# Kernel optimization log

Hardware: AMD Instinct MI355X
Metric: run time of the kernel (lower is better)

Reference implementation:

```python
import jax, jax.numpy as jnp
import numpy as np

B, S, D, H = 2, 2048, 1024, 16
DK = D // H


def setup_inputs() -> dict:
    key = jax.random.key(0)
    ks = jax.random.split(key, 12)
    scale = 0.02
    inp = {
        "query": jax.random.normal(ks[0], (B, S, D), jnp.float32),
        "key_": jax.random.normal(ks[1], (B, S, D), jnp.float32),
        "value": jax.random.normal(ks[2], (B, S, D), jnp.float32),
        # causal mask; masked_fill where mask == 0
        "mask": jnp.tril(jnp.ones((S, S), jnp.int32))[None, None, :, :],
        # torch Linear weights are [out, in]; y = x @ W.T + b
        "Wq": jax.random.normal(ks[3], (D, D), jnp.float32) * scale,
        "bq": jax.random.normal(ks[4], (D,), jnp.float32) * scale,
        "Wk": jax.random.normal(ks[5], (D, D), jnp.float32) * scale,
        "bk": jax.random.normal(ks[6], (D,), jnp.float32) * scale,
        "Wv": jax.random.normal(ks[7], (D, D), jnp.float32) * scale,
        "bv": jax.random.normal(ks[8], (D,), jnp.float32) * scale,
        "Wo": jax.random.normal(ks[9], (D, D), jnp.float32) * scale,
        "bo": jax.random.normal(ks[10], (D,), jnp.float32) * scale,
    }
    return inp


def reference(query, key_, value, mask, Wq, bq, Wk, bk, Wv, bv, Wo, bo):
    # projections (torch Linear: x @ W.T + b)
    Q = query @ Wq.T + bq
    K = key_ @ Wk.T + bk
    V = value @ Wv.T + bv
    # [B, S, D] -> [B, H, S, DK]
    Q = Q.reshape(B, S, H, DK).transpose(0, 2, 1, 3)
    K = K.reshape(B, S, H, DK).transpose(0, 2, 1, 3)
    V = V.reshape(B, S, H, DK).transpose(0, 2, 1, 3)
    scores = jnp.einsum("bhqd,bhkd->bhqk", Q, K) / jnp.sqrt(jnp.float32(DK))
    scores = jnp.where(mask == 0, jnp.float32(-1e9), scores)
    attn = jax.nn.softmax(scores, axis=-1)
    # dropout is identity in eval mode
    context = jnp.einsum("bhqk,bhkd->bhqd", attn, V)
    context = context.transpose(0, 2, 1, 3).reshape(B, S, D)
    output = context @ Wo.T + bo
    return (output, attn)
```

## Files before the change

kernel.cpp:

```cpp
#include <hip/hip_runtime.h>
#include <hip/hip_bf16.h>

#define BB 2
#define SS 2048
#define DD 1024
#define HH 16

typedef __attribute__((ext_vector_type(8))) short bf16x8;
typedef __attribute__((ext_vector_type(4))) float f32x4;
typedef __attribute__((ext_vector_type(4))) unsigned int u32x4;
typedef __attribute__((ext_vector_type(2))) unsigned int u32x2;

__device__ inline unsigned short f2bf(float f) {
  unsigned int u = __float_as_uint(f);
  u += 0x7fff + ((u >> 16) & 1);
  return (unsigned short)(u >> 16);
}

__device__ inline void gll16(const void* g, void* l) {
  __builtin_amdgcn_global_load_lds(
      (const __attribute__((address_space(1))) unsigned int*)g,
      (__attribute__((address_space(3))) unsigned int*)l, 16, 0, 0);
}

__device__ inline int swz(int row, int col) {
  return row * 64 + ((((col >> 3) + row + (row >> 3)) & 7) << 3) + (col & 7);
}

__global__ void convert_all(const float* __restrict__ q, const float* __restrict__ k,
                            const float* __restrict__ v, const float* __restrict__ wq,
                            const float* __restrict__ wk, const float* __restrict__ wv,
                            const float* __restrict__ wo, unsigned short* __restrict__ dst) {
  int gi = blockIdx.x * 256 + threadIdx.x;
  long base = (long)gi * 4;
  if (base >= 16777216L) return;
  const float* src;
  long off;
  if (base < 12582912L) {
    int a = (int)(base >> 22);
    off = base & 4194303L;
    src = (a == 0) ? q : (a == 1 ? k : v);
  } else {
    long wb = base - 12582912L;
    int a = (int)(wb >> 20);
    off = wb & 1048575L;
    src = (a == 0) ? wq : (a == 1 ? wk : (a == 2 ? wv : wo));
  }
  const float4 f = *(const float4*)(src + off);
  ushort4 o;
  o.x = f2bf(f.x); o.y = f2bf(f.y); o.z = f2bf(f.z); o.w = f2bf(f.w);
  *(ushort4*)(dst + base) = o;
}

template <int OUT_F32>
__global__ __launch_bounds__(256, 3) void gemm_bt(const unsigned short* __restrict__ Aall,
                                                  const unsigned short* __restrict__ Wall,
                                                  const float* __restrict__ b0,
                                                  const float* __restrict__ b1,
                                                  const float* __restrict__ b2,
                                                  void* __restrict__ Call) {
  __shared__ unsigned short As[128 * 64];
  __shared__ unsigned short Bs[128 * 64];
  const int tid = threadIdx.x;
  const int lane = tid & 63;
  const int w = tid >> 6;
  const int wm = w >> 1, wn = w & 1;
  const int z = blockIdx.z;
  const int m0 = blockIdx.y * 128;
  const int n0 = blockIdx.x * 128;
  const unsigned short* A = Aall + (long)z * 4194304;
  const unsigned short* W = Wall + (long)z * 1048576;
  const float* bias = (z == 0) ? b0 : (z == 1 ? b1 : b2);
  const int r = lane & 15, g = lane >> 4;
  const int lrow = lane >> 3;
  const int lcol = (lane & 7) * 8;

  f32x4 acc[4][4];
#pragma unroll
  for (int i = 0; i < 4; i++)
#pragma unroll
    for (int j = 0; j < 4; j++) acc[i][j] = (f32x4){0.f, 0.f, 0.f, 0.f};

  for (int kt = 0; kt < 16; kt++) {
    const int k0 = kt * 64;
#pragma unroll
    for (int t = 0; t < 4; t++) {
      int row = w * 32 + t * 8 + lrow;
      gll16(A + (long)(m0 + row) * 1024 + k0 + lcol, &As[(w * 32 + t * 8) * 64]);
      gll16(W + (long)(n0 + row) * 1024 + k0 + lcol, &Bs[(w * 32 + t * 8) * 64]);
    }
    __syncthreads();
#pragma unroll
    for (int kk = 0; kk < 2; kk++) {
      bf16x8 af[4], bfr[4];
#pragma unroll
      for (int mi = 0; mi < 4; mi++)
        af[mi] = *(const bf16x8*)&As[(wm * 64 + mi * 16 + r) * 64 + kk * 32 + g * 8];
#pragma unroll
      for (int ni = 0; ni < 4; ni++)
        bfr[ni] = *(const bf16x8*)&Bs[(wn * 64 + ni * 16 + r) * 64 + kk * 32 + g * 8];
#pragma unroll
      for (int mi = 0; mi < 4; mi++)
#pragma unroll
        for (int ni = 0; ni < 4; ni++)
          acc[mi][ni] = __builtin_amdgcn_mfma_f32_16x16x32_bf16(af[mi], bfr[ni], acc[mi][ni], 0, 0, 0);
    }
    __syncthreads();
  }
#pragma unroll
  for (int ni = 0; ni < 4; ni++) {
    int n = n0 + wn * 64 + ni * 16 + r;
    float bv = bias[n];
#pragma unroll
    for (int mi = 0; mi < 4; mi++) {
      if (OUT_F32) {
#pragma unroll
        for (int reg = 0; reg < 4; reg++) {
          int m = m0 + wm * 64 + mi * 16 + g * 4 + reg;
          ((float*)Call)[(long)m * 1024 + n] = acc[mi][ni][reg] + bv;
        }
      } else if (z == 2) {
        int m = m0 + wm * 64 + mi * 16 + g * 4;
        ushort4 o;
        o.x = f2bf(acc[mi][ni][0] + bv);
        o.y = f2bf(acc[mi][ni][1] + bv);
        o.z = f2bf(acc[mi][ni][2] + bv);
        o.w = f2bf(acc[mi][ni][3] + bv);
        long idx = 2L * 4194304 + ((long)((m >> 11) * 1024 + n)) * 2048 + (m & 2047);
        *(ushort4*)((unsigned short*)Call + idx) = o;
      } else {
#pragma unroll
        for (int reg = 0; reg < 4; reg++) {
          int m = m0 + wm * 64 + mi * 16 + g * 4 + reg;
          ((unsigned short*)Call)[(long)z * 4194304 + (long)m * 1024 + n] =
              f2bf(acc[mi][ni][reg] + bv);
        }
      }
    }
  }
}

__global__ __launch_bounds__(256, 2) void attn_kernel(const unsigned short* __restrict__ Qb,
                                                      const unsigned short* __restrict__ Kb,
                                                      const unsigned short* __restrict__ Vtg,
                                                      unsigned short* __restrict__ Ctx,
                                                      float* __restrict__ attn) {
  __shared__ unsigned short Ps[64 * 64];
  const int tid = threadIdx.x;
  const int lane = tid & 63;
  const int w = tid >> 6;
  const int r = lane & 15, g = lane >> 4;
  const int h = blockIdx.y, b = blockIdx.z;
  const int bh = b * HH + h;
  const unsigned short* Kg = Kb + (long)b * SS * DD + h * 64;
  const unsigned short* Vg = Vtg + (long)bh * 64 * SS;
  float* attn_bh = attn + (long)bh * SS * SS;

  for (int half = 0; half < 2; half++) {
    const int qt = half ? (31 - (int)blockIdx.x) : (int)blockIdx.x;
    const int q0 = qt * 64;
    const unsigned short* Qg = Qb + (long)(b * SS + q0) * DD + h * 64;
    bf16x8 aq0 = *(const bf16x8*)(Qg + (long)(16 * w + r) * DD + g * 8);
    bf16x8 aq1 = *(const bf16x8*)(Qg + (long)(16 * w + r) * DD + 32 + g * 8);

    float rs = 0.f;
    for (int kt = 0; kt <= qt; kt++) {
      const unsigned short* Kt = Kg + (long)kt * 64 * DD;
#pragma unroll
      for (int mi = 0; mi < 4; mi++) {
        bf16x8 ak0 = *(const bf16x8*)(Kt + (long)(mi * 16 + r) * DD + g * 8);
        bf16x8 ak1 = *(const bf16x8*)(Kt + (long)(mi * 16 + r) * DD + 32 + g * 8);
        f32x4 sa = (f32x4){0.f, 0.f, 0.f, 0.f};
        sa = __builtin_amdgcn_mfma_f32_16x16x32_bf16(ak0, aq0, sa, 0, 0, 0);
        sa = __builtin_amdgcn_mfma_f32_16x16x32_bf16(ak1, aq1, sa, 0, 0, 0);
        if (kt == qt) {
#pragma unroll
          for (int reg = 0; reg < 4; reg++)
            rs += (mi * 16 + g * 4 + reg <= 16 * w + r) ? __expf(sa[reg] * 0.125f) : 0.f;
        } else {
#pragma unroll
          for (int reg = 0; reg < 4; reg++) rs += __expf(sa[reg] * 0.125f);
        }
      }
    }
    rs += __shfl_xor(rs, 16);
    rs += __shfl_xor(rs, 32);
    const float inv = 1.f / rs;

    f32x4 oacc[4];
#pragma unroll
    for (int dj = 0; dj < 4; dj++) oacc[dj] = (f32x4){0.f, 0.f, 0.f, 0.f};
    float* rowp = attn_bh + (long)(q0 + 16 * w + r) * SS;
    for (int kt = 0; kt <= qt; kt++) {
      const unsigned short* Kt = Kg + (long)kt * 64 * DD;
#pragma unroll
      for (int mi = 0; mi < 4; mi++) {
        bf16x8 ak0 = *(const bf16x8*)(Kt + (long)(mi * 16 + r) * DD + g * 8);
        bf16x8 ak1 = *(const bf16x8*)(Kt + (long)(mi * 16 + r) * DD + 32 + g * 8);
        f32x4 sa = (f32x4){0.f, 0.f, 0.f, 0.f};
        sa = __builtin_amdgcn_mfma_f32_16x16x32_bf16(ak0, aq0, sa, 0, 0, 0);
        sa = __builtin_amdgcn_mfma_f32_16x16x32_bf16(ak1, aq1, sa, 0, 0, 0);
        f32x4 p;
        if (kt == qt) {
#pragma unroll
          for (int reg = 0; reg < 4; reg++)
            p[reg] = (mi * 16 + g * 4 + reg <= 16 * w + r) ? __expf(sa[reg] * 0.125f) * inv : 0.f;
        } else {
#pragma unroll
          for (int reg = 0; reg < 4; reg++) p[reg] = __expf(sa[reg] * 0.125f) * inv;
        }
        *(f32x4*)(rowp + kt * 64 + mi * 16 + g * 4) = p;
        unsigned int p01 = (unsigned)f2bf(p[0]) | ((unsigned)f2bf(p[1]) << 16);
        unsigned int p23 = (unsigned)f2bf(p[2]) | ((unsigned)f2bf(p[3]) << 16);
        *(u32x2*)&Ps[swz(16 * w + r, mi * 16 + g * 4)] = (u32x2){p01, p23};
      }
#pragma unroll
      for (int kk = 0; kk < 2; kk++) {
        bf16x8 ap = *(const bf16x8*)&Ps[swz(16 * w + r, kk * 32 + g * 8)];
#pragma unroll
        for (int dj = 0; dj < 4; dj++) {
          bf16x8 bv = *(const bf16x8*)(Vg + (long)(dj * 16 + r) * SS + kt * 64 + kk * 32 + g * 8);
          oacc[dj] = __builtin_amdgcn_mfma_f32_16x16x32_bf16(ap, bv, oacc[dj], 0, 0, 0);
        }
      }
    }
#pragma unroll
    for (int dj = 0; dj < 4; dj++) {
#pragma unroll
      for (int reg = 0; reg < 4; reg++) {
        int rowg = q0 + 16 * w + g * 4 + reg;
        Ctx[(long)(b * SS + rowg) * DD + h * 64 + dj * 16 + r] = f2bf(oacc[dj][reg]);
      }
    }
    int zs = (qt + 1) * 64;
    if (zs < SS) {
      int zc = SS - zs;
      f32x4 zero = (f32x4){0.f, 0.f, 0.f, 0.f};
      for (int rr = 0; rr < 64; rr++) {
        float* rp = attn_bh + (long)(q0 + rr) * SS + zs;
        for (int cc = tid * 4; cc < zc; cc += 1024) *(f32x4*)(rp + cc) = zero;
      }
    }
  }
}

extern "C" void kernel_launch(void* const* d_in, const int* in_sizes, int n_in,
                              void* d_out, int out_size, void* d_ws, size_t ws_size,
                              hipStream_t stream) {
  const float* q  = (const float*)d_in[0];
  const float* k  = (const float*)d_in[1];
  const float* v  = (const float*)d_in[2];
  const float* wq = (const float*)d_in[4];
  const float* bq = (const float*)d_in[5];
  const float* wk = (const float*)d_in[6];
  const float* bk = (const float*)d_in[7];
  const float* wv = (const float*)d_in[8];
  const float* bv = (const float*)d_in[9];
  const float* wo = (const float*)d_in[10];
  const float* bo = (const float*)d_in[11];

  unsigned short* ws = (unsigned short*)d_ws;
  unsigned short* Xq  = ws;
  unsigned short* Wqb = ws + 12582912;
  unsigned short* Qb  = ws + 16777216;
  unsigned short* Ctx = ws + 29360128;
  float* outp = (float*)d_out;
  float* attn = outp + 4194304;

  convert_all<<<dim3(16384), dim3(256), 0, stream>>>(q, k, v, wq, wk, wv, wo, ws);
  gemm_bt<0><<<dim3(8, 32, 3), dim3(256), 0, stream>>>(Xq, Wqb, bq, bk, bv, (void*)Qb);
  attn_kernel<<<dim3(16, 16, 2), dim3(256), 0, stream>>>(Qb, Qb + 4194304, Qb + 8388608, Ctx, attn);
  gemm_bt<1><<<dim3(8, 32, 1), dim3(256), 0, stream>>>(Ctx, Wqb + 3145728, bo, bo, bo, (void*)outp);
}
```

Before: 858.6 us.

## Stage K and V tiles in double-buffered LDS with register prefetch

The attention kernel now loads each 64x64 K tile (and V tile in the second pass) cooperatively into swizzled shared memory, double-buffered, while prefetching the next tile into registers. MFMA operands then come from LDS instead of every wave issuing redundant global loads, which cuts global/L2 traffic across the four waves. Launch bounds are raised to 3 blocks per CU to keep occupancy up. It adds a barrier per K tile and extra LDS use. The attention output is an fp32 matrix with causal zero fill, so that memory traffic may dominate anyway.

```diff
diff --git a/kernel.cpp b/kernel.cpp
--- a/kernel.cpp
+++ b/kernel.cpp
@@ -140,11 +140,13 @@
   }
 }
 
-__global__ __launch_bounds__(256, 2) void attn_kernel(const unsigned short* __restrict__ Qb,
+__global__ __launch_bounds__(256, 3) void attn_kernel(const unsigned short* __restrict__ Qb,
                                                       const unsigned short* __restrict__ Kb,
                                                       const unsigned short* __restrict__ Vtg,
                                                       unsigned short* __restrict__ Ctx,
                                                       float* __restrict__ attn) {
+  __shared__ unsigned short Ks[2][64 * 64];
+  __shared__ unsigned short Vs[2][64 * 64];
   __shared__ unsigned short Ps[64 * 64];
   const int tid = threadIdx.x;
   const int lane = tid & 63;
@@ -155,6 +157,8 @@
   const unsigned short* Kg = Kb + (long)b * SS * DD + h * 64;
   const unsigned short* Vg = Vtg + (long)bh * 64 * SS;
   float* attn_bh = attn + (long)bh * SS * SS;
+  const int srow = tid >> 3;
+  const int scg = tid & 7;
 
   for (int half = 0; half < 2; half++) {
     const int qt = half ? (31 - (int)blockIdx.x) : (int)blockIdx.x;
@@ -163,13 +167,26 @@
     bf16x8 aq0 = *(const bf16x8*)(Qg + (long)(16 * w + r) * DD + g * 8);
     bf16x8 aq1 = *(const bf16x8*)(Qg + (long)(16 * w + r) * DD + 32 + g * 8);
 
+    u32x4 kpre[2];
+#pragma unroll
+    for (int it = 0; it < 2; it++)
+      kpre[it] = *(const u32x4*)(Kg + (long)(it * 32 + srow) * DD + scg * 8);
+    __syncthreads();
     float rs = 0.f;
     for (int kt = 0; kt <= qt; kt++) {
-      const unsigned short* Kt = Kg + (long)kt * 64 * DD;
+      unsigned short* kbuf = Ks[kt & 1];
+#pragma unroll
+      for (int it = 0; it < 2; it++)
+        *(u32x4*)&kbuf[swz(it * 32 + srow, scg * 8)] = kpre[it];
+      const int ktn = (kt < qt) ? kt + 1 : kt;
+#pragma unroll
+      for (int it = 0; it < 2; it++)
+        kpre[it] = *(const u32x4*)(Kg + (long)(ktn * 64 + it * 32 + srow) * DD + scg * 8);
+      __syncthreads();
 #pragma unroll
       for (int mi = 0; mi < 4; mi++) {
-        bf16x8 ak0 = *(const bf16x8*)(Kt + (long)(mi * 16 + r) * DD + g * 8);
-        bf16x8 ak1 = *(const bf16x8*)(Kt + (long)(mi * 16 + r) * DD + 32 + g * 8);
+        bf16x8 ak0 = *(const bf16x8*)&kbuf[swz(mi * 16 + r, g * 8)];
+        bf16x8 ak1 = *(const bf16x8*)&kbuf[swz(mi * 16 + r, 32 + g * 8)];
         f32x4 sa = (f32x4){0.f, 0.f, 0.f, 0.f};
         sa = __builtin_amdgcn_mfma_f32_16x16x32_bf16(ak0, aq0, sa, 0, 0, 0);
         sa = __builtin_amdgcn_mfma_f32_16x16x32_bf16(ak1, aq1, sa, 0, 0, 0);
@@ -190,13 +207,33 @@
     f32x4 oacc[4];
 #pragma unroll
     for (int dj = 0; dj < 4; dj++) oacc[dj] = (f32x4){0.f, 0.f, 0.f, 0.f};
+    u32x4 vpre[2];
+#pragma unroll
+    for (int it = 0; it < 2; it++) {
+      kpre[it] = *(const u32x4*)(Kg + (long)(it * 32 + srow) * DD + scg * 8);
+      vpre[it] = *(const u32x4*)(Vg + (long)(it * 32 + srow) * SS + scg * 8);
+    }
+    __syncthreads();
     float* rowp = attn_bh + (long)(q0 + 16 * w + r) * SS;
     for (int kt = 0; kt <= qt; kt++) {
-      const unsigned short* Kt = Kg + (long)kt * 64 * DD;
+      unsigned short* kbuf = Ks[kt & 1];
+      unsigned short* vbuf = Vs[kt & 1];
+#pragma unroll
+      for (int it = 0; it < 2; it++) {
+        *(u32x4*)&kbuf[swz(it * 32 + srow, scg * 8)] = kpre[it];
+        *(u32x4*)&vbuf[swz(it * 32 + srow, scg * 8)] = vpre[it];
+      }
+      const int ktn = (kt < qt) ? kt + 1 : kt;
+#pragma unroll
+      for (int it = 0; it < 2; it++) {
+        kpre[it] = *(const u32x4*)(Kg + (long)(ktn * 64 + it * 32 + srow) * DD + scg * 8);
+        vpre[it] = *(const u32x4*)(Vg + (long)(it * 32 + srow) * SS + ktn * 64 + scg * 8);
+      }
+      __syncthreads();
 #pragma unroll
       for (int mi = 0; mi < 4; mi++) {
-        bf16x8 ak0 = *(const bf16x8*)(Kt + (long)(mi * 16 + r) * DD + g * 8);
-        bf16x8 ak1 = *(const bf16x8*)(Kt + (long)(mi * 16 + r) * DD + 32 + g * 8);
+        bf16x8 ak0 = *(const bf16x8*)&kbuf[swz(mi * 16 + r, g * 8)];
+        bf16x8 ak1 = *(const bf16x8*)&kbuf[swz(mi * 16 + r, 32 + g * 8)];
         f32x4 sa = (f32x4){0.f, 0.f, 0.f, 0.f};
         sa = __builtin_amdgcn_mfma_f32_16x16x32_bf16(ak0, aq0, sa, 0, 0, 0);
         sa = __builtin_amdgcn_mfma_f32_16x16x32_bf16(ak1, aq1, sa, 0, 0, 0);
@@ -219,7 +256,7 @@
         bf16x8 ap = *(const bf16x8*)&Ps[swz(16 * w + r, kk * 32 + g * 8)];
 #pragma unroll
         for (int dj = 0; dj < 4; dj++) {
-          bf16x8 bv = *(const bf16x8*)(Vg + (long)(dj * 16 + r) * SS + kt * 64 + kk * 32 + g * 8);
+          bf16x8 bv = *(const bf16x8*)&vbuf[swz(dj * 16 + r, kk * 32 + g * 8)];
           oacc[dj] = __builtin_amdgcn_mfma_f32_16x16x32_bf16(ap, bv, oacc[dj], 0, 0, 0);
         }
       }
```

Result: faster. 738.3 us (-14.0%).
